# Kernel optimization log

Measured on AMD Instinct MI355X. Metric: run time of the kernel, lower is better.

## Reference

```python
import jax, jax.numpy as jnp
import numpy as np

B, N, T = 64, 100, 100
FS, F, STRIDE = 3, 16, 1  # filter_size, num_filters, stride
DENSITY = 0.05


def setup_inputs() -> dict:
    key = jax.random.key(0)
    k1, k2, k3, k4 = jax.random.split(key, 4)
    vals = jax.random.uniform(k1, (B, N, N, T), dtype=jnp.float32, minval=0.01, maxval=1.0)
    mask = jax.random.uniform(k2, (B, N, N, T)) < DENSITY
    x = jnp.where(mask, vals, 0.0)
    # learned params, matching tf.random_normal_initializer(stddev=0.05)
    w = 0.05 * jax.random.normal(k3, (N * N * FS, F), dtype=jnp.float32)
    gammat = 0.05 * jax.random.normal(k4, (1, 1), dtype=jnp.float32)
    return {"x": x, "w": w, "gammat": gammat}


def reference(x, w, gammat):
    # gamma = (gamma_max - gamma_min) * sigmoid(gammat) + gamma_min, gamma_max=10
    gamma = 10.0 * jax.nn.sigmoid(gammat[0, 0])
    # tf.sparse.map_values(exp, -gamma*x): only nonzero entries are exponentiated
    xs = jnp.where(x != 0, jnp.exp(-gamma * x), 0.0)
    # windowed sparse-dense matmul over time == 1D conv over T with channels N*N
    xc = xs.reshape(B, N * N, T)                         # (B, NN, T)
    # w flattening order is ((i*N + j)*FS + dt) -> reshape (NN, FS, F)
    kern = w.reshape(N * N, FS, F).transpose(2, 0, 1)    # (F, NN, FS)
    out = jax.lax.conv_general_dilated(
        xc, kern, window_strides=(STRIDE,), padding="VALID",
        dimension_numbers=("NCH", "OIH", "NCH"))          # (B, F, T-FS+1)
    return out[:, :, None, :]                            # (B, F, 1, outT)
```

## Files before the change

kernel.cpp:

```cpp
#include <hip/hip_runtime.h>

#define BB     64
#define NNCH   10000
#define TOUT   98
#define FF     16
#define CPB    64
#define NCHUNK 157
#define EP     106
#define WP     200
#define ACCN   (TOUT * FF)

typedef __attribute__((ext_vector_type(8))) short s8v;
typedef __attribute__((ext_vector_type(4))) float f4v;

__device__ __forceinline__ ushort bf_rne(float v) {
    unsigned b = __float_as_uint(v);
    return (ushort)((b + 0x7FFFu + ((b >> 16) & 1u)) >> 16);
}

__global__ __launch_bounds__(256) void tgcnn_mfma(
    const float* __restrict__ x,
    const float* __restrict__ w,
    const float* __restrict__ gammat,
    float* __restrict__ ws,
    int nco, int ch)
{
    __shared__ __align__(16) ushort E[CPB + 1][EP];
    __shared__ __align__(16) ushort W[FF][WP];

    const int tid = threadIdx.x;
    const int bid = blockIdx.x;
    const int b   = bid / nco;
    const int co  = bid - b * nco;

    const float gt    = gammat[0];
    const float gamma = 10.0f / (1.0f + __expf(-gt));
    const float kk    = -gamma * 1.4426950408889634f;

    const int wave = tid >> 6, lane = tid & 63;
    const int tcol = lane & 15;
    const int kb   = lane >> 4;
    const int tile0 = wave, tile1 = wave + 4;
    const bool two  = (tile1 < 7);

    f4v acc0 = {0.f, 0.f, 0.f, 0.f};
    f4v acc1 = {0.f, 0.f, 0.f, 0.f};

    const float4* x4  = (const float4*)x;
    const float4* wg4 = (const float4*)w;

    for (int kc = 0; kc < ch; ++kc) {
        const int cs = co * ch + kc;
        if (cs >= NCHUNK) break;
        const int cbase = cs * CPB;

        if (kc) __syncthreads();

        for (int i = tid; i < CPB * 25; i += 256) {
            const int cl = i / 25, q = i - cl * 25;
            const int c  = cbase + cl;
            float4 v = make_float4(0.f, 0.f, 0.f, 0.f);
            if (c < NNCH) v = x4[((size_t)b * NNCH + c) * 25 + q];
            const unsigned e0 = (v.x != 0.f) ? bf_rne(exp2f(kk * v.x)) : 0;
            const unsigned e1 = (v.y != 0.f) ? bf_rne(exp2f(kk * v.y)) : 0;
            const unsigned e2 = (v.z != 0.f) ? bf_rne(exp2f(kk * v.z)) : 0;
            const unsigned e3 = (v.w != 0.f) ? bf_rne(exp2f(kk * v.w)) : 0;
            *(unsigned*)&E[cl][q * 4 + 0] = e0 | (e1 << 16);
            *(unsigned*)&E[cl][q * 4 + 2] = e2 | (e3 << 16);
        }

        for (int i = tid; i < CPB * 12; i += 256) {
            const int cl = i / 12, r = i - cl * 12;
            const int c  = cbase + cl;
            float4 wv = make_float4(0.f, 0.f, 0.f, 0.f);
            if (c < NNCH) wv = wg4[(size_t)c * 12 + r];
            const int dt = r >> 2, fq = (r & 3) * 4, kp = dt * CPB + cl;
            W[fq + 0][kp] = bf_rne(wv.x);
            W[fq + 1][kp] = bf_rne(wv.y);
            W[fq + 2][kp] = bf_rne(wv.z);
            W[fq + 3][kp] = bf_rne(wv.w);
        }
        __syncthreads();

        #pragma unroll
        for (int ks = 0; ks < 6; ++ks) {
            const int dt = ks >> 1;
            const int cb = (ks & 1) * 32 + kb * 8;

            const s8v bfrag = *(const s8v*)&W[tcol][ks * 32 + kb * 8];

            {
                const int trow = tile0 * 16 + tcol + dt;
                s8v afrag;
                #pragma unroll
                for (int j = 0; j < 8; ++j) afrag[j] = (short)E[cb + j][trow];
                acc0 = __builtin_amdgcn_mfma_f32_16x16x32_bf16(afrag, bfrag, acc0, 0, 0, 0);
            }
            if (two) {
                const int trow = tile1 * 16 + tcol + dt;
                s8v afrag;
                #pragma unroll
                for (int j = 0; j < 8; ++j) afrag[j] = (short)E[cb + j][trow];
                acc1 = __builtin_amdgcn_mfma_f32_16x16x32_bf16(afrag, bfrag, acc1, 0, 0, 0);
            }
        }
    }

    float* wsb = ws + ((size_t)co * BB + b) * ACCN;
    const int f = lane & 15;
    const int rbase = (lane >> 4) * 4;
    #pragma unroll
    for (int r = 0; r < 4; ++r) {
        const int m = tile0 * 16 + rbase + r;
        if (m < TOUT) wsb[m * FF + f] = acc0[r];
    }
    if (two) {
        #pragma unroll
        for (int r = 0; r < 4; ++r) {
            const int m = tile1 * 16 + rbase + r;
            if (m < TOUT) wsb[m * FF + f] = acc1[r];
        }
    }
}

__global__ __launch_bounds__(256) void tgcnn_finalize(
    const float* __restrict__ ws, float* __restrict__ out, int nco)
{
    int i = blockIdx.x * 256 + threadIdx.x;
    if (i >= BB * FF * TOUT) return;
    int t = i % TOUT;
    int f = (i / TOUT) & (FF - 1);
    int b = i / (FF * TOUT);
    float s = 0.f;
    for (int co = 0; co < nco; ++co)
        s += ws[((size_t)co * BB + b) * ACCN + t * FF + f];
    out[i] = s;
}

extern "C" void kernel_launch(void* const* d_in, const int* in_sizes, int n_in,
                              void* d_out, int out_size, void* d_ws, size_t ws_size,
                              hipStream_t stream) {
    const float* x = (const float*)d_in[0];
    const float* w = (const float*)d_in[1];
    const float* g = (const float*)d_in[2];
    float* ws = (float*)d_ws;

    const size_t slot = (size_t)BB * ACCN * sizeof(float);
    int navail = (int)(ws_size / slot);
    int nco = navail < 1 ? 1 : (navail > 40 ? 40 : navail);
    int ch  = (NCHUNK + nco - 1) / nco;

    tgcnn_mfma<<<BB * nco, 256, 0, stream>>>(x, w, g, ws, nco, ch);
    tgcnn_finalize<<<(BB * FF * TOUT + 255) / 256, 256, 0, stream>>>(
        ws, (float*)d_out, nco);
}
```

Before: 89.82 us.

## Launch one block per chunk and reduce partial sums with atomics

Each block now handles a single 64-channel chunk, giving BB*NCHUNK blocks, and its partial result is added into one zeroed workspace with atomicAdd instead of being written to per-split slots that finalize sums. The MFMA loop reuses each A fragment across the three filter taps by keeping three accumulators and shifting the output index on store. The LDS layouts are also repacked with new pitches. This raises parallelism and removes the multi-slot reduction, at the cost of many float atomics on the same addresses, an added memset, and nondeterministic summation order.

```diff
diff --git a/kernel.cpp b/kernel.cpp
--- a/kernel.cpp
+++ b/kernel.cpp
@@ -6,8 +6,8 @@
 #define FF     16
 #define CPB    64
 #define NCHUNK 157
-#define EP     106
-#define WP     200
+#define EPITCH 102
+#define WLP    72
 #define ACCN   (TOUT * FF)
 
 typedef __attribute__((ext_vector_type(8))) short s8v;
@@ -18,45 +18,31 @@
     return (ushort)((b + 0x7FFFu + ((b >> 16) & 1u)) >> 16);
 }
 
-__global__ __launch_bounds__(256) void tgcnn_mfma(
+__global__ __launch_bounds__(256) void tgcnn_gemm(
     const float* __restrict__ x,
     const float* __restrict__ w,
     const float* __restrict__ gammat,
-    float* __restrict__ ws,
-    int nco, int ch)
+    float* __restrict__ ws)
 {
-    __shared__ __align__(16) ushort E[CPB + 1][EP];
-    __shared__ __align__(16) ushort W[FF][WP];
+    __shared__ __align__(16) ushort E[CPB * EPITCH + 16];
+    __shared__ __align__(16) ushort WL[3][FF][WLP];
 
     const int tid = threadIdx.x;
     const int bid = blockIdx.x;
-    const int b   = bid / nco;
-    const int co  = bid - b * nco;
+    const int b   = bid / NCHUNK;
+    const int cs  = bid - b * NCHUNK;
+    const int cbase = cs * CPB;
 
     const float gt    = gammat[0];
     const float gamma = 10.0f / (1.0f + __expf(-gt));
     const float kk    = -gamma * 1.4426950408889634f;
 
-    const int wave = tid >> 6, lane = tid & 63;
-    const int tcol = lane & 15;
-    const int kb   = lane >> 4;
-    const int tile0 = wave, tile1 = wave + 4;
-    const bool two  = (tile1 < 7);
-
-    f4v acc0 = {0.f, 0.f, 0.f, 0.f};
-    f4v acc1 = {0.f, 0.f, 0.f, 0.f};
-
-    const float4* x4  = (const float4*)x;
-    const float4* wg4 = (const float4*)w;
-
-    for (int kc = 0; kc < ch; ++kc) {
-        const int cs = co * ch + kc;
-        if (cs >= NCHUNK) break;
-        const int cbase = cs * CPB;
-
-        if (kc) __syncthreads();
-
-        for (int i = tid; i < CPB * 25; i += 256) {
+    const float4* x4 = (const float4*)x;
+    unsigned* e32 = (unsigned*)E;
+    #pragma unroll
+    for (int rr = 0; rr < 7; ++rr) {
+        const int i = rr * 256 + tid;
+        if (i < CPB * 25) {
             const int cl = i / 25, q = i - cl * 25;
             const int c  = cbase + cl;
             float4 v = make_float4(0.f, 0.f, 0.f, 0.f);
@@ -65,76 +51,96 @@
             const unsigned e1 = (v.y != 0.f) ? bf_rne(exp2f(kk * v.y)) : 0;
             const unsigned e2 = (v.z != 0.f) ? bf_rne(exp2f(kk * v.z)) : 0;
             const unsigned e3 = (v.w != 0.f) ? bf_rne(exp2f(kk * v.w)) : 0;
-            *(unsigned*)&E[cl][q * 4 + 0] = e0 | (e1 << 16);
-            *(unsigned*)&E[cl][q * 4 + 2] = e2 | (e3 << 16);
-        }
-
-        for (int i = tid; i < CPB * 12; i += 256) {
-            const int cl = i / 12, r = i - cl * 12;
-            const int c  = cbase + cl;
-            float4 wv = make_float4(0.f, 0.f, 0.f, 0.f);
-            if (c < NNCH) wv = wg4[(size_t)c * 12 + r];
-            const int dt = r >> 2, fq = (r & 3) * 4, kp = dt * CPB + cl;
-            W[fq + 0][kp] = bf_rne(wv.x);
-            W[fq + 1][kp] = bf_rne(wv.y);
-            W[fq + 2][kp] = bf_rne(wv.z);
-            W[fq + 3][kp] = bf_rne(wv.w);
-        }
-        __syncthreads();
-
-        #pragma unroll
-        for (int ks = 0; ks < 6; ++ks) {
-            const int dt = ks >> 1;
-            const int cb = (ks & 1) * 32 + kb * 8;
-
-            const s8v bfrag = *(const s8v*)&W[tcol][ks * 32 + kb * 8];
-
-            {
-                const int trow = tile0 * 16 + tcol + dt;
-                s8v afrag;
-                #pragma unroll
-                for (int j = 0; j < 8; ++j) afrag[j] = (short)E[cb + j][trow];
-                acc0 = __builtin_amdgcn_mfma_f32_16x16x32_bf16(afrag, bfrag, acc0, 0, 0, 0);
-            }
-            if (two) {
-                const int trow = tile1 * 16 + tcol + dt;
-                s8v afrag;
-                #pragma unroll
-                for (int j = 0; j < 8; ++j) afrag[j] = (short)E[cb + j][trow];
-                acc1 = __builtin_amdgcn_mfma_f32_16x16x32_bf16(afrag, bfrag, acc1, 0, 0, 0);
-            }
+            const int wd = cl * 51 + 2 * q;
+            e32[wd]     = e0 | (e1 << 16);
+            e32[wd + 1] = e2 | (e3 << 16);
         }
     }
 
-    float* wsb = ws + ((size_t)co * BB + b) * ACCN;
+    const float4* wg4 = (const float4*)w;
+    #pragma unroll
+    for (int rr = 0; rr < 3; ++rr) {
+        const int i  = rr * 256 + tid;
+        const int cl = i / 12, r = i - cl * 12;
+        const int c  = cbase + cl;
+        float4 wv = make_float4(0.f, 0.f, 0.f, 0.f);
+        if (c < NNCH) wv = wg4[(size_t)c * 12 + r];
+        const int dt = r >> 2, f0 = (r & 3) * 4;
+        WL[dt][f0 + 0][cl] = bf_rne(wv.x);
+        WL[dt][f0 + 1][cl] = bf_rne(wv.y);
+        WL[dt][f0 + 2][cl] = bf_rne(wv.z);
+        WL[dt][f0 + 3][cl] = bf_rne(wv.w);
+    }
+    __syncthreads();
+
+    const int wave = tid >> 6, lane = tid & 63;
+    const int tcol = lane & 15;
+    const int kb   = lane >> 4;
+    const int tile0 = wave, tile1 = wave + 4;
+    const bool two  = (tile1 < 7);
+    const int tau0 = tile0 * 16 + tcol;
+    const int tau1 = tile1 * 16 + tcol;
+
+    f4v acc0[3] = {{0.f,0.f,0.f,0.f},{0.f,0.f,0.f,0.f},{0.f,0.f,0.f,0.f}};
+    f4v acc1[3] = {{0.f,0.f,0.f,0.f},{0.f,0.f,0.f,0.f},{0.f,0.f,0.f,0.f}};
+
+    #pragma unroll
+    for (int ks = 0; ks < 2; ++ks) {
+        const int cb = ks * 32 + kb * 8;
+
+        s8v a0, a1;
+        #pragma unroll
+        for (int j = 0; j < 8; ++j) a0[j] = (short)E[(cb + j) * EPITCH + tau0];
+        if (two) {
+            #pragma unroll
+            for (int j = 0; j < 8; ++j) a1[j] = (short)E[(cb + j) * EPITCH + tau1];
+        }
+
+        #pragma unroll
+        for (int dt = 0; dt < 3; ++dt) {
+            const s8v bf = *(const s8v*)&WL[dt][tcol][cb];
+            acc0[dt] = __builtin_amdgcn_mfma_f32_16x16x32_bf16(a0, bf, acc0[dt], 0, 0, 0);
+            if (two)
+                acc1[dt] = __builtin_amdgcn_mfma_f32_16x16x32_bf16(a1, bf, acc1[dt], 0, 0, 0);
+        }
+    }
+
+    float* wsb = ws + (size_t)b * ACCN;
     const int f = lane & 15;
     const int rbase = (lane >> 4) * 4;
     #pragma unroll
     for (int r = 0; r < 4; ++r) {
-        const int m = tile0 * 16 + rbase + r;
-        if (m < TOUT) wsb[m * FF + f] = acc0[r];
+        const int m0 = tile0 * 16 + rbase + r;
+        #pragma unroll
+        for (int dt = 0; dt < 3; ++dt) {
+            const int t = m0 - dt;
+            if ((unsigned)t < (unsigned)TOUT)
+                atomicAdd(&wsb[t * FF + f], acc0[dt][r]);
+        }
     }
     if (two) {
         #pragma unroll
         for (int r = 0; r < 4; ++r) {
-            const int m = tile1 * 16 + rbase + r;
-            if (m < TOUT) wsb[m * FF + f] = acc1[r];
+            const int m1 = tile1 * 16 + rbase + r;
+            #pragma unroll
+            for (int dt = 0; dt < 3; ++dt) {
+                const int t = m1 - dt;
+                if ((unsigned)t < (unsigned)TOUT)
+                    atomicAdd(&wsb[t * FF + f], acc1[dt][r]);
+            }
         }
     }
 }
 
 __global__ __launch_bounds__(256) void tgcnn_finalize(
-    const float* __restrict__ ws, float* __restrict__ out, int nco)
+    const float* __restrict__ ws, float* __restrict__ out)
 {
     int i = blockIdx.x * 256 + threadIdx.x;
     if (i >= BB * FF * TOUT) return;
     int t = i % TOUT;
     int f = (i / TOUT) & (FF - 1);
     int b = i / (FF * TOUT);
-    float s = 0.f;
-    for (int co = 0; co < nco; ++co)
-        s += ws[((size_t)co * BB + b) * ACCN + t * FF + f];
-    out[i] = s;
+    out[i] = ws[(size_t)b * ACCN + t * FF + f];
 }
 
 extern "C" void kernel_launch(void* const* d_in, const int* in_sizes, int n_in,
@@ -145,12 +151,8 @@
     const float* g = (const float*)d_in[2];
     float* ws = (float*)d_ws;
 
-    const size_t slot = (size_t)BB * ACCN * sizeof(float);
-    int navail = (int)(ws_size / slot);
-    int nco = navail < 1 ? 1 : (navail > 40 ? 40 : navail);
-    int ch  = (NCHUNK + nco - 1) / nco;
-
-    tgcnn_mfma<<<BB * nco, 256, 0, stream>>>(x, w, g, ws, nco, ch);
+    hipMemsetAsync(d_ws, 0, (size_t)BB * ACCN * sizeof(float), stream);
+    tgcnn_gemm<<<BB * NCHUNK, 256, 0, stream>>>(x, w, g, ws);
     tgcnn_finalize<<<(BB * FF * TOUT + 255) / 256, 256, 0, stream>>>(
-        ws, (float*)d_out, nco);
+        ws, (float*)d_out);
 }
```

Measured after the change: 192.9 us. 2.15x slower.
